# Optimization experiments

Measured on AMD Instinct MI355X. Metric: run time of the kernel, lower is better.

## Reference

```python
import jax, jax.numpy as jnp
import numpy as np

C = 1.0  # Poincare ball curvature
EPS = 4e-3       # float32 boundary epsilon (hgcn convention)
MIN_NORM = 1e-15


def _norm(x):
    return jnp.maximum(jnp.linalg.norm(x, axis=-1, keepdims=True), MIN_NORM)


def proj(x, c=C):
    # clip points to the open ball of radius (1-eps)/sqrt(c)
    maxnorm = (1.0 - EPS) / jnp.sqrt(c)
    n = _norm(x)
    return jnp.where(n > maxnorm, x / n * maxnorm, x)


def logmap0(x, c=C):
    sqrt_c = jnp.sqrt(c)
    n = _norm(x)
    arg = jnp.clip(sqrt_c * n, -1.0 + 1e-7, 1.0 - 1e-7)
    return x / n * jnp.arctanh(arg) / sqrt_c


def expmap0(u, c=C):
    sqrt_c = jnp.sqrt(c)
    n = _norm(u)
    return jnp.tanh(sqrt_c * n) * u / (sqrt_c * n)


def setup_inputs() -> dict:
    key = jax.random.key(0)
    k1, k2 = jax.random.split(key)
    N, D_IN, D_OUT = 8192, 4096, 4096
    # points inside the unit ball: small-scale gaussian (norm ~ 0.01*sqrt(4096) ~ 0.64)
    x = jax.random.normal(k1, (N, D_IN), dtype=jnp.float32) * 0.01
    # xavier_uniform with gain=sqrt(2)
    bound = np.sqrt(2.0) * np.sqrt(6.0 / (D_IN + D_OUT))
    W = jax.random.uniform(k2, (D_OUT, D_IN), dtype=jnp.float32, minval=-bound, maxval=bound)
    b = jnp.zeros((D_OUT,), dtype=jnp.float32)
    return {"x": x, "W": W, "b": b}


def reference(x, W, b):
    # CustomHyperbolicLinear (euc_tangent_fc path, activation=Identity):
    # logmap0 -> dense linear -> expmap0 -> proj
    t = logmap0(x)
    t = t @ W.T + b
    y = proj(expmap0(t))
    # outer activation: CustomHyperbolicActivation(Tanh)
    # proj -> logmap0 -> tanh -> proj_tan0 (identity on Poincare) -> expmap0 -> proj
    y = proj(y)
    t2 = jnp.tanh(logmap0(y))
    out = proj(expmap0(t2))
    return out
```

## Files before the change

kernel.cpp:

```cpp
#include <hip/hip_runtime.h>
#include <stdint.h>
#include <math.h>

#define GM 8192
#define GN 4096
#define GK 4096
#define BM 128
#define BN 128
#define BK 32

typedef __bf16 bf16x8 __attribute__((ext_vector_type(8)));
typedef float  f32x4  __attribute__((ext_vector_type(4)));

typedef const __attribute__((address_space(1))) void* gas_ptr;
typedef __attribute__((address_space(3))) void* las_ptr;

__device__ __forceinline__ unsigned short f2bf(float f) {
    union { float f; unsigned u; } a; a.f = f;
    unsigned r = a.u + 0x7FFFu + ((a.u >> 16) & 1u);
    return (unsigned short)(r >> 16);
}

__device__ __forceinline__ float fast_tanh(float x) {
    float xc = fminf(fmaxf(x, -15.f), 15.f);
    float e = __expf(2.f * xc);
    return (e - 1.f) * __builtin_amdgcn_rcpf(e + 1.f);
}
__device__ __forceinline__ float fast_atanh(float x) {
    return 0.5f * __logf((1.f + x) * __builtin_amdgcn_rcpf(1.f - x));
}

__global__ __launch_bounds__(256) void pre_kernel(const float* __restrict__ x,
                                                  const float* __restrict__ W,
                                                  unsigned short* __restrict__ t,
                                                  unsigned short* __restrict__ Wb) {
    const int b = blockIdx.x;
    const int tid = threadIdx.x;
    if (b < GM) {
        __shared__ float red[4];
        const float* xr = x + (size_t)b * GK;
        float v[16];
        float ss = 0.f;
#pragma unroll
        for (int j = 0; j < 4; ++j) {
            f32x4 p = *(const f32x4*)(xr + (size_t)(tid + j * 256) * 4);
#pragma unroll
            for (int e = 0; e < 4; ++e) { v[j * 4 + e] = p[e]; ss += p[e] * p[e]; }
        }
#pragma unroll
        for (int off = 32; off; off >>= 1) ss += __shfl_down(ss, off);
        if ((tid & 63) == 0) red[tid >> 6] = ss;
        __syncthreads();
        ss = red[0] + red[1] + red[2] + red[3];
        const float n = fmaxf(sqrtf(ss), 1e-15f);
        const float scale = fast_atanh(fminf(n, 1.f - 1e-7f)) * __builtin_amdgcn_rcpf(n);
        unsigned short* tr = t + (size_t)b * GK;
#pragma unroll
        for (int j = 0; j < 4; ++j) {
            ushort4 o;
            o.x = f2bf(v[j * 4 + 0] * scale);
            o.y = f2bf(v[j * 4 + 1] * scale);
            o.z = f2bf(v[j * 4 + 2] * scale);
            o.w = f2bf(v[j * 4 + 3] * scale);
            *(ushort4*)(tr + (size_t)(tid + j * 256) * 4) = o;
        }
    } else {
        const int r = b - GM;
        const float* wr = W + (size_t)r * GK;
        unsigned short* wo = Wb + (size_t)r * GK;
#pragma unroll
        for (int j = 0; j < 4; ++j) {
            f32x4 p = *(const f32x4*)(wr + (size_t)(tid + j * 256) * 4);
            ushort4 o;
            o.x = f2bf(p[0]); o.y = f2bf(p[1]); o.z = f2bf(p[2]); o.w = f2bf(p[3]);
            *(ushort4*)(wo + (size_t)(tid + j * 256) * 4) = o;
        }
    }
}

__global__ __launch_bounds__(256, 4) void gemm_kernel(const unsigned short* __restrict__ A,
                                                      const unsigned short* __restrict__ B,
                                                      float* __restrict__ C) {
    __shared__ __align__(16) unsigned short lA[BM * BK];
    __shared__ __align__(16) unsigned short lB[BN * BK];

    const int tid  = threadIdx.x;
    const int wave = tid >> 6;
    const int lane = tid & 63;
    const int m16  = lane & 15;
    const int quad = lane >> 4;
    const int waveM = (wave >> 1) * 64;
    const int waveN = (wave & 1) * 64;
    const int tileM = blockIdx.y * BM;
    const int tileN = blockIdx.x * BN;

    const int rA = lane >> 2;
    const int kg = (lane & 3) * 8;

    const unsigned short* aPtr = A + (size_t)(tileM + wave * 32 + rA) * GK + kg;
    const unsigned short* bPtr = B + (size_t)(tileN + wave * 32 + rA) * GK + kg;
    las_ptr ldsA = (las_ptr)&lA[wave * 1024];
    las_ptr ldsB = (las_ptr)&lB[wave * 1024];

    f32x4 acc[4][4] = {};

#pragma unroll 1
    for (int k0 = 0; k0 < GK; k0 += BK) {
        __builtin_amdgcn_global_load_lds((gas_ptr)(aPtr + k0),                    ldsA, 16, 0, 0);
        __builtin_amdgcn_global_load_lds((gas_ptr)(aPtr + k0 + (size_t)16 * GK),  (las_ptr)((char*)ldsA + 1024), 16, 0, 0);
        __builtin_amdgcn_global_load_lds((gas_ptr)(bPtr + k0),                    ldsB, 16, 0, 0);
        __builtin_amdgcn_global_load_lds((gas_ptr)(bPtr + k0 + (size_t)16 * GK),  (las_ptr)((char*)ldsB + 1024), 16, 0, 0);
        __syncthreads();

        bf16x8 af[4], bfr[4];
#pragma unroll
        for (int i = 0; i < 4; ++i) {
            af[i]  = *(const bf16x8*)&lA[(waveM + i * 16 + m16) * BK + quad * 8];
            bfr[i] = *(const bf16x8*)&lB[(waveN + i * 16 + m16) * BK + quad * 8];
        }
#pragma unroll
        for (int mi = 0; mi < 4; ++mi)
#pragma unroll
            for (int ni = 0; ni < 4; ++ni)
                acc[mi][ni] = __builtin_amdgcn_mfma_f32_16x16x32_bf16(af[mi], bfr[ni], acc[mi][ni], 0, 0, 0);
        __syncthreads();
    }

#pragma unroll
    for (int mi = 0; mi < 4; ++mi)
#pragma unroll
        for (int ni = 0; ni < 4; ++ni)
#pragma unroll
            for (int r = 0; r < 4; ++r) {
                const int row = tileM + waveM + mi * 16 + quad * 4 + r;
                const int col = tileN + waveN + ni * 16 + m16;
                C[(size_t)row * GN + col] = acc[mi][ni][r];
            }
}

__global__ __launch_bounds__(256) void epilogue_kernel(float* __restrict__ C,
                                                       const float* __restrict__ bias) {
    __shared__ float red1[4];
    __shared__ float red2[4];
    const int row = blockIdx.x;
    const int tid = threadIdx.x;
    float* cr = C + (size_t)row * GN;
    float u[16];
    float ss = 0.f;
#pragma unroll
    for (int j = 0; j < 4; ++j) {
        f32x4 p = *(const f32x4*)(cr + (size_t)(tid + j * 256) * 4);
        f32x4 bb = *(const f32x4*)(bias + (size_t)(tid + j * 256) * 4);
#pragma unroll
        for (int e = 0; e < 4; ++e) { float q = p[e] + bb[e]; u[j * 4 + e] = q; ss += q * q; }
    }
#pragma unroll
    for (int off = 32; off; off >>= 1) ss += __shfl_down(ss, off);
    if ((tid & 63) == 0) red1[tid >> 6] = ss;
    __syncthreads();
    ss = red1[0] + red1[1] + red1[2] + red1[3];

    const float n1 = fmaxf(sqrtf(ss), 1e-15f);
    const float ny = fminf(fast_tanh(n1), 0.996f);
    const float g = (ny * __builtin_amdgcn_rcpf(n1)) *
                    (fast_atanh(ny) * __builtin_amdgcn_rcpf(fmaxf(ny, 1e-15f)));

    float t2[16];
    float ss2 = 0.f;
#pragma unroll
    for (int i = 0; i < 16; ++i) { float q = fast_tanh(u[i] * g); t2[i] = q; ss2 += q * q; }
#pragma unroll
    for (int off = 32; off; off >>= 1) ss2 += __shfl_down(ss2, off);
    if ((tid & 63) == 0) red2[tid >> 6] = ss2;
    __syncthreads();
    ss2 = red2[0] + red2[1] + red2[2] + red2[3];

    const float n3 = fmaxf(sqrtf(ss2), 1e-15f);
    const float s3 = fminf(fast_tanh(n3), 0.996f) * __builtin_amdgcn_rcpf(n3);
#pragma unroll
    for (int j = 0; j < 4; ++j) {
        f32x4 o;
#pragma unroll
        for (int e = 0; e < 4; ++e) o[e] = t2[j * 4 + e] * s3;
        *(f32x4*)(cr + (size_t)(tid + j * 256) * 4) = o;
    }
}

extern "C" void kernel_launch(void* const* d_in, const int* in_sizes, int n_in,
                              void* d_out, int out_size, void* d_ws, size_t ws_size,
                              hipStream_t stream) {
    const float* x = (const float*)d_in[0];
    const float* W = (const float*)d_in[1];
    const float* b = (const float*)d_in[2];
    float* out = (float*)d_out;

    unsigned short* t_bf = (unsigned short*)d_ws;
    unsigned short* W_bf = t_bf + (size_t)GM * GK;

    pre_kernel<<<GM + GN, 256, 0, stream>>>(x, W, t_bf, W_bf);
    gemm_kernel<<<dim3(GN / BN, GM / BM), 256, 0, stream>>>(t_bf, W_bf, out);
    epilogue_kernel<<<GM, 256, 0, stream>>>(out, b);
}
```

Before: 590.3 us.

## Store GEMM output as bf16 in workspace and use wave-per-row reductions

The GEMM can now write its intermediate result as bf16 into the workspace instead of fp32, which halves the write and re-read traffic of the large intermediate matrix. The epilogue reads that bf16 buffer and writes the final fp32 output. The pre and epilogue kernels now give each wave its own row and use xor shuffles, which removes shared-memory reductions and block barriers. Rounding the pre-activation values to bf16 adds error, and the bf16 path runs only when the workspace is large enough.

```diff
diff --git a/kernel.cpp b/kernel.cpp
--- a/kernel.cpp
+++ b/kernel.cpp
@@ -20,6 +20,10 @@
     unsigned r = a.u + 0x7FFFu + ((a.u >> 16) & 1u);
     return (unsigned short)(r >> 16);
 }
+__device__ __forceinline__ float bf2f(unsigned short h) {
+    union { unsigned u; float f; } a; a.u = ((unsigned)h) << 16;
+    return a.f;
+}
 
 __device__ __forceinline__ float fast_tanh(float x) {
     float xc = fminf(fmaxf(x, -15.f), 15.f);
@@ -34,53 +38,51 @@
                                                   const float* __restrict__ W,
                                                   unsigned short* __restrict__ t,
                                                   unsigned short* __restrict__ Wb) {
-    const int b = blockIdx.x;
-    const int tid = threadIdx.x;
-    if (b < GM) {
-        __shared__ float red[4];
-        const float* xr = x + (size_t)b * GK;
-        float v[16];
+    const int lane = threadIdx.x & 63;
+    const int wv   = threadIdx.x >> 6;
+    if (blockIdx.x < 2048) {
+        const int row = blockIdx.x * 4 + wv;
+        const float* xr = x + (size_t)row * GK;
+        float v[64];
         float ss = 0.f;
 #pragma unroll
-        for (int j = 0; j < 4; ++j) {
-            f32x4 p = *(const f32x4*)(xr + (size_t)(tid + j * 256) * 4);
+        for (int j = 0; j < 16; ++j) {
+            f32x4 p = *(const f32x4*)(xr + (size_t)(j * 64 + lane) * 4);
 #pragma unroll
             for (int e = 0; e < 4; ++e) { v[j * 4 + e] = p[e]; ss += p[e] * p[e]; }
         }
 #pragma unroll
-        for (int off = 32; off; off >>= 1) ss += __shfl_down(ss, off);
-        if ((tid & 63) == 0) red[tid >> 6] = ss;
-        __syncthreads();
-        ss = red[0] + red[1] + red[2] + red[3];
+        for (int off = 32; off; off >>= 1) ss += __shfl_xor(ss, off);
         const float n = fmaxf(sqrtf(ss), 1e-15f);
         const float scale = fast_atanh(fminf(n, 1.f - 1e-7f)) * __builtin_amdgcn_rcpf(n);
-        unsigned short* tr = t + (size_t)b * GK;
-#pragma unroll
-        for (int j = 0; j < 4; ++j) {
+        unsigned short* tr = t + (size_t)row * GK;
+#pragma unroll
+        for (int j = 0; j < 16; ++j) {
             ushort4 o;
             o.x = f2bf(v[j * 4 + 0] * scale);
             o.y = f2bf(v[j * 4 + 1] * scale);
             o.z = f2bf(v[j * 4 + 2] * scale);
             o.w = f2bf(v[j * 4 + 3] * scale);
-            *(ushort4*)(tr + (size_t)(tid + j * 256) * 4) = o;
+            *(ushort4*)(tr + (size_t)(j * 64 + lane) * 4) = o;
         }
     } else {
-        const int r = b - GM;
-        const float* wr = W + (size_t)r * GK;
-        unsigned short* wo = Wb + (size_t)r * GK;
-#pragma unroll
-        for (int j = 0; j < 4; ++j) {
-            f32x4 p = *(const f32x4*)(wr + (size_t)(tid + j * 256) * 4);
+        const int row = (blockIdx.x - 2048) * 4 + wv;
+        const float* wr = W + (size_t)row * GK;
+        unsigned short* wo = Wb + (size_t)row * GK;
+#pragma unroll 4
+        for (int j = 0; j < 16; ++j) {
+            f32x4 p = *(const f32x4*)(wr + (size_t)(j * 64 + lane) * 4);
             ushort4 o;
             o.x = f2bf(p[0]); o.y = f2bf(p[1]); o.z = f2bf(p[2]); o.w = f2bf(p[3]);
-            *(ushort4*)(wo + (size_t)(tid + j * 256) * 4) = o;
-        }
-    }
-}
-
+            *(ushort4*)(wo + (size_t)(j * 64 + lane) * 4) = o;
+        }
+    }
+}
+
+template <bool BF16C>
 __global__ __launch_bounds__(256, 4) void gemm_kernel(const unsigned short* __restrict__ A,
                                                       const unsigned short* __restrict__ B,
-                                                      float* __restrict__ C) {
+                                                      void* __restrict__ Cv) {
     __shared__ __align__(16) unsigned short lA[BM * BK];
     __shared__ __align__(16) unsigned short lB[BN * BK];
 
@@ -106,10 +108,10 @@
 
 #pragma unroll 1
     for (int k0 = 0; k0 < GK; k0 += BK) {
-        __builtin_amdgcn_global_load_lds((gas_ptr)(aPtr + k0),                    ldsA, 16, 0, 0);
-        __builtin_amdgcn_global_load_lds((gas_ptr)(aPtr + k0 + (size_t)16 * GK),  (las_ptr)((char*)ldsA + 1024), 16, 0, 0);
-        __builtin_amdgcn_global_load_lds((gas_ptr)(bPtr + k0),                    ldsB, 16, 0, 0);
-        __builtin_amdgcn_global_load_lds((gas_ptr)(bPtr + k0 + (size_t)16 * GK),  (las_ptr)((char*)ldsB + 1024), 16, 0, 0);
+        __builtin_amdgcn_global_load_lds((gas_ptr)(aPtr + k0),                   ldsA, 16, 0, 0);
+        __builtin_amdgcn_global_load_lds((gas_ptr)(aPtr + k0 + (size_t)16 * GK), (las_ptr)((char*)ldsA + 1024), 16, 0, 0);
+        __builtin_amdgcn_global_load_lds((gas_ptr)(bPtr + k0),                   ldsB, 16, 0, 0);
+        __builtin_amdgcn_global_load_lds((gas_ptr)(bPtr + k0 + (size_t)16 * GK), (las_ptr)((char*)ldsB + 1024), 16, 0, 0);
         __syncthreads();
 
         bf16x8 af[4], bfr[4];
@@ -134,55 +136,60 @@
             for (int r = 0; r < 4; ++r) {
                 const int row = tileM + waveM + mi * 16 + quad * 4 + r;
                 const int col = tileN + waveN + ni * 16 + m16;
-                C[(size_t)row * GN + col] = acc[mi][ni][r];
+                if (BF16C)
+                    ((unsigned short*)Cv)[(size_t)row * GN + col] = f2bf(acc[mi][ni][r]);
+                else
+                    ((float*)Cv)[(size_t)row * GN + col] = acc[mi][ni][r];
             }
 }
 
-__global__ __launch_bounds__(256) void epilogue_kernel(float* __restrict__ C,
-                                                       const float* __restrict__ bias) {
-    __shared__ float red1[4];
-    __shared__ float red2[4];
-    const int row = blockIdx.x;
-    const int tid = threadIdx.x;
-    float* cr = C + (size_t)row * GN;
-    float u[16];
+template <bool BF16C>
+__global__ __launch_bounds__(256) void epilogue_kernel(const void* __restrict__ Cv,
+                                                       const float* __restrict__ bias,
+                                                       float* __restrict__ out) {
+    const int lane = threadIdx.x & 63;
+    const int row  = blockIdx.x * 4 + (threadIdx.x >> 6);
+    float u[64];
     float ss = 0.f;
 #pragma unroll
-    for (int j = 0; j < 4; ++j) {
-        f32x4 p = *(const f32x4*)(cr + (size_t)(tid + j * 256) * 4);
-        f32x4 bb = *(const f32x4*)(bias + (size_t)(tid + j * 256) * 4);
-#pragma unroll
-        for (int e = 0; e < 4; ++e) { float q = p[e] + bb[e]; u[j * 4 + e] = q; ss += q * q; }
-    }
-#pragma unroll
-    for (int off = 32; off; off >>= 1) ss += __shfl_down(ss, off);
-    if ((tid & 63) == 0) red1[tid >> 6] = ss;
-    __syncthreads();
-    ss = red1[0] + red1[1] + red1[2] + red1[3];
+    for (int j = 0; j < 16; ++j) {
+        const size_t col = (size_t)(j * 64 + lane) * 4;
+        f32x4 bb = *(const f32x4*)(bias + col);
+        if (BF16C) {
+            ushort4 p = *(const ushort4*)((const unsigned short*)Cv + (size_t)row * GN + col);
+            float q0 = bf2f(p.x) + bb[0], q1 = bf2f(p.y) + bb[1];
+            float q2 = bf2f(p.z) + bb[2], q3 = bf2f(p.w) + bb[3];
+            u[j * 4 + 0] = q0; u[j * 4 + 1] = q1; u[j * 4 + 2] = q2; u[j * 4 + 3] = q3;
+            ss += q0 * q0 + q1 * q1 + q2 * q2 + q3 * q3;
+        } else {
+            f32x4 p = *(const f32x4*)((const float*)Cv + (size_t)row * GN + col);
+#pragma unroll
+            for (int e = 0; e < 4; ++e) { float q = p[e] + bb[e]; u[j * 4 + e] = q; ss += q * q; }
+        }
+    }
+#pragma unroll
+    for (int off = 32; off; off >>= 1) ss += __shfl_xor(ss, off);
 
     const float n1 = fmaxf(sqrtf(ss), 1e-15f);
     const float ny = fminf(fast_tanh(n1), 0.996f);
     const float g = (ny * __builtin_amdgcn_rcpf(n1)) *
                     (fast_atanh(ny) * __builtin_amdgcn_rcpf(fmaxf(ny, 1e-15f)));
 
-    float t2[16];
     float ss2 = 0.f;
 #pragma unroll
-    for (int i = 0; i < 16; ++i) { float q = fast_tanh(u[i] * g); t2[i] = q; ss2 += q * q; }
-#pragma unroll
-    for (int off = 32; off; off >>= 1) ss2 += __shfl_down(ss2, off);
-    if ((tid & 63) == 0) red2[tid >> 6] = ss2;
-    __syncthreads();
-    ss2 = red2[0] + red2[1] + red2[2] + red2[3];
+    for (int i = 0; i < 64; ++i) { float q = fast_tanh(u[i] * g); u[i] = q; ss2 += q * q; }
+#pragma unroll
+    for (int off = 32; off; off >>= 1) ss2 += __shfl_xor(ss2, off);
 
     const float n3 = fmaxf(sqrtf(ss2), 1e-15f);
     const float s3 = fminf(fast_tanh(n3), 0.996f) * __builtin_amdgcn_rcpf(n3);
-#pragma unroll
-    for (int j = 0; j < 4; ++j) {
+    float* orow = out + (size_t)row * GN;
+#pragma unroll
+    for (int j = 0; j < 16; ++j) {
         f32x4 o;
 #pragma unroll
-        for (int e = 0; e < 4; ++e) o[e] = t2[j * 4 + e] * s3;
-        *(f32x4*)(cr + (size_t)(tid + j * 256) * 4) = o;
+        for (int e = 0; e < 4; ++e) o[e] = u[j * 4 + e] * s3;
+        *(f32x4*)(orow + (size_t)(j * 64 + lane) * 4) = o;
     }
 }
 
@@ -196,8 +203,16 @@
 
     unsigned short* t_bf = (unsigned short*)d_ws;
     unsigned short* W_bf = t_bf + (size_t)GM * GK;
-
-    pre_kernel<<<GM + GN, 256, 0, stream>>>(x, W, t_bf, W_bf);
-    gemm_kernel<<<dim3(GN / BN, GM / BM), 256, 0, stream>>>(t_bf, W_bf, out);
-    epilogue_kernel<<<GM, 256, 0, stream>>>(out, b);
-}
+    unsigned short* C_bf = W_bf + (size_t)GN * GK;
+    const size_t need_bf16c = ((size_t)GM * GK + (size_t)GN * GK + (size_t)GM * GN) * 2;
+    const bool bf16c = ws_size >= need_bf16c;
+
+    pre_kernel<<<2048 + 1024, 256, 0, stream>>>(x, W, t_bf, W_bf);
+    if (bf16c) {
+        gemm_kernel<true><<<dim3(GN / BN, GM / BM), 256, 0, stream>>>(t_bf, W_bf, (void*)C_bf);
+        epilogue_kernel<true><<<2048, 256, 0, stream>>>((const void*)C_bf, b, out);
+    } else {
+        gemm_kernel<false><<<dim3(GN / BN, GM / BM), 256, 0, stream>>>(t_bf, W_bf, (void*)out);
+        epilogue_kernel<false><<<2048, 256, 0, stream>>>((const void*)out, b, out);
+    }
+}
```

Measured after the change: 590.2 us. No clear change (-0.0%).
